# Kernel optimization log

Hardware: AMD Instinct MI355X
Metric: run time of the kernel (lower is better)

## Reference

```python
import jax, jax.numpy as jnp
import numpy as np

B_TREES, NARY, HS, NHEAD, NLVL = 16, 3, 512, 2, 6
EDIM = 352
LN_EPS = 1e-5

def _build_structure():
    # forest of B_TREES perfect ternary trees, depth NLVL; nodes numbered leaves-first, level-major
    off, o = {}, 0
    for l in range(NLVL - 1, -1, -1):
        off[l] = o
        o += B_TREES * 3 ** l
    node_ids = [off[l] + np.arange(B_TREES * 3 ** l) for l in range(NLVL)]
    child_idx = {}
    for l in range(NLVL - 1):
        m = 3 ** l
        t = np.repeat(np.arange(B_TREES), m)
        p = np.tile(np.arange(m), B_TREES)
        base = off[l + 1] + t * (3 ** (l + 1)) + 3 * p
        child_idx[l] = base[:, None] + np.arange(NARY)[None, :]
    return o, node_ids, child_idx

N_NODES, NODE_IDS, CHILD_IDX = _build_structure()

def _ln(x, w, b):
    mu = x.mean(-1, keepdims=True)
    var = x.var(-1, keepdims=True)
    return (x - mu) / jnp.sqrt(var + LN_EPS) * w + b

def _mha(x, wqkv, bqkv, wo, bo):
    # x: [S, B, H]; torch MHA with batch_first=False (seq dim 0, as in reduce_func)
    S, B, H = x.shape
    hd = H // NHEAD
    q, k, v = jnp.split(x @ wqkv.T + bqkv, 3, axis=-1)
    q = q.reshape(S, B, NHEAD, hd)
    k = k.reshape(S, B, NHEAD, hd)
    v = v.reshape(S, B, NHEAD, hd)
    scores = jnp.einsum('sbnd,tbnd->bnst', q, k) / jnp.sqrt(jnp.asarray(hd, x.dtype))
    attn = jax.nn.softmax(scores, axis=-1)
    o = jnp.einsum('bnst,tbnd->sbnd', attn, v).reshape(S, B, H)
    return o @ wo.T + bo

def _transformer(x, qkv_w, qkv_b, out_w, out_b, ln1_w, ln1_b, ff1_w, ff1_b, ff2_w, ff2_b, ln2_w, ln2_b):
    # 2 post-norm TransformerEncoderLayers, relu FF, dropout off (eval)
    for i in range(2):
        x = _ln(x + _mha(x, qkv_w[i], qkv_b[i], out_w[i], out_b[i]), ln1_w[i], ln1_b[i])
        ff = jax.nn.relu(x @ ff1_w[i].T + ff1_b[i]) @ ff2_w[i].T + ff2_b[i]
        x = _ln(x + ff, ln2_w[i], ln2_b[i])
    return x

def _forward(floats, ints):
    (user_emb, poi_emb, cat_emb, coo_emb, time_pos, W_iou, U_iou, b_iou,
     W_f, U_f, b_f, qkv_w, qkv_b, out_w, out_b, ln1_w, ln1_b, ff1_w, ff1_b,
     ff2_w, ff2_b, ln2_w, ln2_b, dec_poi_w, dec_poi_b, dec_cat_w, dec_cat_b,
     dec_coo_w, dec_coo_b) = floats
    user_ids, poi_ids, cat_ids, coo_ids, time_ids, mask = ints
    mi = mask.astype(jnp.int32)
    x = jnp.concatenate([user_emb[user_ids * mi], poi_emb[poi_ids * mi],
                         cat_emb[cat_ids * mi], coo_emb[coo_ids * mi]], axis=1)
    x = x + 0.5 * time_pos[time_ids * mi]
    x = x * mask.astype(x.dtype)[:, None]  # embed_dropout is identity in eval; per-node mask
    h = jnp.zeros((N_NODES, HS), x.dtype)
    c = jnp.zeros((N_NODES, HS), x.dtype)
    # leaves: reduce never fires -> iou stays at W_iou(x) (no b_iou), c = 0
    leaf = NODE_IDS[NLVL - 1]
    i0, o0, u0 = jnp.split(x[leaf] @ W_iou.T, 3, axis=1)
    c_leaf = jax.nn.sigmoid(i0) * jnp.tanh(u0)
    h = h.at[leaf].set(jax.nn.sigmoid(o0) * jnp.tanh(c_leaf))
    c = c.at[leaf].set(c_leaf)
    # topological propagation, bottom-up level frontiers
    for l in range(NLVL - 2, -1, -1):
        idx = NODE_IDS[l]
        ci = CHILD_IDX[l]
        m = idx.shape[0]
        h_ch = h[ci]  # mailbox gather [m, nary, HS]
        c_ch = c[ci]
        xl = x[idx]
        Wx = jnp.tile(xl @ W_f.T, (1, NARY))
        f = jax.nn.sigmoid(Wx + h_ch.reshape(m, NARY * HS) @ U_f.T + jnp.tile(b_f, (1, NARY)))
        h_att = _transformer(h_ch, qkv_w, qkv_b, out_w, out_b, ln1_w, ln1_b,
                             ff1_w, ff1_b, ff2_w, ff2_b, ln2_w, ln2_b)
        iou = xl @ W_iou.T + h_att.reshape(m, NARY * HS) @ U_iou.T + b_iou
        c_red = jnp.sum(f.reshape(m, NARY, HS) * c_ch, axis=1)
        i1, o1, u1 = jnp.split(iou, 3, axis=1)
        c_new = jax.nn.sigmoid(i1) * jnp.tanh(u1) + c_red
        h_new = jax.nn.sigmoid(o1) * jnp.tanh(c_new)
        h = h.at[idx].set(h_new)
        c = c.at[idx].set(c_new)
    # model_dropout identity in eval
    y_poi = h @ dec_poi_w.T + dec_poi_b
    y_cat = h @ dec_cat_w.T + dec_cat_b
    y_coo = h @ dec_coo_w.T + dec_coo_b
    return y_poi, y_cat, y_coo

def setup_inputs():
    key = jax.random.key(0)
    ks = iter(jax.random.split(key, 64))
    def rn(shape, s=0.05):
        return jax.random.normal(next(ks), shape, dtype=jnp.float32) * s
    def ri(shape, hi):
        return jax.random.randint(next(ks), shape, 0, hi, dtype=jnp.int32)
    N = N_NODES
    return dict(
        user_ids=ri([N], 3000), poi_ids=ri([N], 5000), cat_ids=ri([N], 300),
        coo_ids=ri([N], 1024), time_ids=ri([N], 96), mask=ri([N], 2),
        user_emb=rn([3000, 128], 0.02), poi_emb=rn([5000, 128], 0.02),
        cat_emb=rn([300, 32], 0.02), coo_emb=rn([1024, 64], 0.02),
        time_pos=rn([96, EDIM], 0.02),
        W_iou=rn([3 * HS, EDIM]), U_iou=rn([3 * HS, NARY * HS]), b_iou=jnp.zeros((1, 3 * HS)),
        W_f=rn([HS, EDIM]), U_f=rn([NARY * HS, NARY * HS]), b_f=jnp.zeros((1, HS)),
        qkv_w=rn([2, 3 * HS, HS]), qkv_b=jnp.zeros((2, 3 * HS)),
        out_w=rn([2, HS, HS]), out_b=jnp.zeros((2, HS)),
        ln1_w=jnp.ones((2, HS)), ln1_b=jnp.zeros((2, HS)),
        ff1_w=rn([2, HS, HS]), ff1_b=jnp.zeros((2, HS)),
        ff2_w=rn([2, HS, HS]), ff2_b=jnp.zeros((2, HS)),
        ln2_w=jnp.ones((2, HS)), ln2_b=jnp.zeros((2, HS)),
        dec_poi_w=rn([5000, HS]), dec_poi_b=jnp.zeros((5000,)),
        dec_cat_w=rn([300, HS]), dec_cat_b=jnp.zeros((300,)),
        dec_coo_w=rn([1024, HS]), dec_coo_b=jnp.zeros((1024,)),
    )

def reference(user_ids, poi_ids, cat_ids, coo_ids, time_ids, mask,
              user_emb, poi_emb, cat_emb, coo_emb, time_pos,
              W_iou, U_iou, b_iou, W_f, U_f, b_f,
              qkv_w, qkv_b, out_w, out_b, ln1_w, ln1_b, ff1_w, ff1_b,
              ff2_w, ff2_b, ln2_w, ln2_b,
              dec_poi_w, dec_poi_b, dec_cat_w, dec_cat_b, dec_coo_w, dec_coo_b):
    floats = (user_emb, poi_emb, cat_emb, coo_emb, time_pos, W_iou, U_iou, b_iou,
              W_f, U_f, b_f, qkv_w, qkv_b, out_w, out_b, ln1_w, ln1_b, ff1_w, ff1_b,
              ff2_w, ff2_b, ln2_w, ln2_b, dec_poi_w, dec_poi_b, dec_cat_w, dec_cat_b,
              dec_coo_w, dec_coo_b)
    ints = (user_ids, poi_ids, cat_ids, coo_ids, time_ids, mask)
    return _forward(floats, ints)
```

## Files before the change

kernel.cpp:

```cpp
#include <hip/hip_runtime.h>
#include <hip/hip_bf16.h>


namespace {

constexpr int NN = 5824;
constexpr int ED = 352;

typedef __bf16 bf16;
typedef short s16x8 __attribute__((ext_vector_type(8)));
typedef float f32x4 __attribute__((ext_vector_type(4)));

__device__ __forceinline__ float sigmoidf_(float x) { return 1.f / (1.f + expf(-x)); }

__device__ __forceinline__ void gload_lds16(const void* g, void* s) {
  __builtin_amdgcn_global_load_lds(
      (const __attribute__((address_space(1))) unsigned int*)g,
      (__attribute__((address_space(3))) unsigned int*)s, 16, 0, 0);
}

template <int MODE, bool DUAL, bool BPAIR, bool BF32, bool PIPE>
__global__ __launch_bounds__(256) void bgemm_k(
    const bf16* __restrict__ A, const bf16* __restrict__ Alo,
    const bf16* __restrict__ Bh_, const bf16* __restrict__ Bl_,
    const float* __restrict__ Bf0, const float* __restrict__ Bf1,
    const float* __restrict__ Bf2,
    void* __restrict__ Cp, bf16* __restrict__ Clo, const float* __restrict__ Cacc,
    const float* __restrict__ bias, const float* __restrict__ bias1,
    const float* __restrict__ bias2, bf16* __restrict__ VTout, int mpad,
    int M, int N, int K, int lda, int ldb, int ldc, float alpha,
    long long sA1, long long sA2, long long sB1, long long sB2,
    long long sC1, long long sC2, int nh) {
  const int bz = blockIdx.z;
  const int b1 = bz / nh, b2 = bz - b1 * nh;
  A += (long long)b1 * sA1 + (long long)b2 * sA2;
  if (DUAL) Alo += (long long)b1 * sA1 + (long long)b2 * sA2;
  if (!BF32) {
    Bh_ += (long long)b1 * sB1 + (long long)b2 * sB2;
    if (BPAIR) Bl_ += (long long)b1 * sB1 + (long long)b2 * sB2;
  }
  const long long coff = (long long)b1 * sC1 + (long long)b2 * sC2;
  const int bm = blockIdx.y * 128, bn = blockIdx.x * 128;

  constexpr int NSTG = PIPE ? 2 : 1;
  __shared__ bf16 As[NSTG][128 * 32];
  __shared__ bf16 Ls[DUAL ? NSTG : 1][DUAL ? 128 * 32 : 8];
  __shared__ bf16 Bh[NSTG][128 * 32];
  __shared__ bf16 Bl[BPAIR ? NSTG : 1][BPAIR ? 128 * 32 : 8];
  const int tid = threadIdx.x;
  const int l = tid & 63;
  const int wr = ((tid >> 7) & 1) * 64;
  const int wc = ((tid >> 6) & 1) * 64;
  f32x4 acc[4][4];
#pragma unroll
  for (int i = 0; i < 4; ++i)
#pragma unroll
    for (int j = 0; j < 4; ++j) acc[i][j] = (f32x4){0.f, 0.f, 0.f, 0.f};

  auto STAGE = [&](int st, int k0) {
#pragma unroll
    for (int r = 0; r < 2; ++r) {
      int idx = r * 256 + tid;
      int row = idx >> 2, cs = idx & 3;
      int cg = cs ^ (row & 3);
      int ra = bm + row; if (ra > M - 1) ra = M - 1;
      int rb = bn + row; if (rb > N - 1) rb = N - 1;
      gload_lds16(A + (long long)ra * lda + k0 + cg * 8, &As[st][idx * 8]);
      if (DUAL) gload_lds16(Alo + (long long)ra * lda + k0 + cg * 8, &Ls[st][idx * 8]);
      if (BF32) {
        const float* src;
        if (rb < 5000)      src = Bf0 + (long long)rb * ldb + k0 + cg * 8;
        else if (rb < 5300) src = Bf1 + (long long)(rb - 5000) * ldb + k0 + cg * 8;
        else                src = Bf2 + (long long)(rb - 5300) * ldb + k0 + cg * 8;
        float4 x = *reinterpret_cast<const float4*>(src);
        float4 y = *reinterpret_cast<const float4*>(src + 4);
        float w[8] = {x.x, x.y, x.z, x.w, y.x, y.y, y.z, y.w};
        bf16 hb_[8], lb_[8];
#pragma unroll
        for (int q = 0; q < 8; ++q) {
          bf16 hq = (bf16)w[q];
          hb_[q] = hq;
          lb_[q] = (bf16)(w[q] - (float)hq);
        }
        *reinterpret_cast<s16x8*>(&Bh[st][idx * 8]) = *reinterpret_cast<s16x8*>(hb_);
        if (BPAIR)
          *reinterpret_cast<s16x8*>(&Bl[st][idx * 8]) = *reinterpret_cast<s16x8*>(lb_);
      } else {
        gload_lds16(Bh_ + (long long)rb * ldb + k0 + cg * 8, &Bh[st][idx * 8]);
        if (BPAIR) gload_lds16(Bl_ + (long long)rb * ldb + k0 + cg * 8, &Bl[st][idx * 8]);
      }
    }
  };

  auto COMPUTE = [&](int st) {
    s16x8 af[4], al[4], bh4[4], bl4[4];
#pragma unroll
    for (int mi = 0; mi < 4; ++mi) {
      int row = wr + mi * 16 + (l & 15);
      int ch = ((l >> 4) ^ row) & 3;
      af[mi] = *reinterpret_cast<const s16x8*>(&As[st][row * 32 + ch * 8]);
      if (DUAL) al[mi] = *reinterpret_cast<const s16x8*>(&Ls[st][row * 32 + ch * 8]);
    }
#pragma unroll
    for (int ni = 0; ni < 4; ++ni) {
      int row = wc + ni * 16 + (l & 15);
      int ch = ((l >> 4) ^ row) & 3;
      bh4[ni] = *reinterpret_cast<const s16x8*>(&Bh[st][row * 32 + ch * 8]);
      if (BPAIR) bl4[ni] = *reinterpret_cast<const s16x8*>(&Bl[st][row * 32 + ch * 8]);
    }
#pragma unroll
    for (int mi = 0; mi < 4; ++mi)
#pragma unroll
      for (int ni = 0; ni < 4; ++ni) {
        acc[mi][ni] =
            __builtin_amdgcn_mfma_f32_16x16x32_bf16(af[mi], bh4[ni], acc[mi][ni], 0, 0, 0);
        if (BPAIR)
          acc[mi][ni] =
              __builtin_amdgcn_mfma_f32_16x16x32_bf16(af[mi], bl4[ni], acc[mi][ni], 0, 0, 0);
        if (DUAL)
          acc[mi][ni] =
              __builtin_amdgcn_mfma_f32_16x16x32_bf16(al[mi], bh4[ni], acc[mi][ni], 0, 0, 0);
      }
  };

  if (!PIPE) {
    for (int k0 = 0; k0 < K; k0 += 32) {
      STAGE(0, k0);
      __syncthreads();
      COMPUTE(0);
      __syncthreads();
    }
  } else {
    STAGE(0, 0);
    asm volatile("s_waitcnt vmcnt(0)" ::: "memory");
    __builtin_amdgcn_s_barrier();
    int cur = 0;
    for (int k0 = 0; k0 < K; k0 += 32) {
      if (k0 + 32 < K) STAGE(cur ^ 1, k0 + 32);
      COMPUTE(cur);
      asm volatile("s_waitcnt vmcnt(0)" ::: "memory");
      __builtin_amdgcn_sched_barrier(0);
      __builtin_amdgcn_s_barrier();
      cur ^= 1;
    }
  }

  const int lc = l & 15, lr4 = (l >> 4) * 4;
#pragma unroll
  for (int mi = 0; mi < 4; ++mi) {
#pragma unroll
    for (int j = 0; j < 4; ++j) {
      int r = bm + wr + mi * 16 + lr4 + j;
      if (MODE != 7 && r >= M) continue;
#pragma unroll
      for (int ni = 0; ni < 4; ++ni) {
        int c = bn + wc + ni * 16 + lc;
        if (c >= N) continue;
        float v = alpha * acc[mi][ni][j];
        if (MODE == 6) {
          v += (c < 5000) ? bias[c] : (c < 5300) ? bias1[c - 5000] : bias2[c - 5300];
        } else if (bias) {
          v += bias[c];
        }
        long long idx = coff + (long long)r * ldc + c;
        if (MODE == 7) {
          if (c >= 1024 && r < 3 * mpad) {
            bf16 pv = (r < M) ? (bf16)v : (bf16)0.f;
            int r3 = r % 3, s = r / 3;
            int hh = (c - 1024) >> 8, n = (c - 1024) & 255;
            VTout[(long long)((r3 * 2 + hh) * 256 + n) * mpad + s] = pv;
          }
          if (r < M) ((bf16*)Cp)[idx] = (bf16)v;
        } else if (MODE == 5) {
          ((float*)Cp)[idx] = v + Cacc[idx];
        } else if (MODE == 0) {
          ((float*)Cp)[idx] = v;
        } else if (MODE == 3) {
          ((bf16*)Cp)[idx] = (bf16)v;
        } else if (MODE == 4) {
          v = fmaxf(v, 0.f);
          bf16 hv = (bf16)v;
          ((bf16*)Cp)[idx] = hv;
          Clo[idx] = (bf16)(v - (float)hv);
        } else {
          float* o0 = (float*)Cp;
          if (c < 5000)      o0[(long long)r * 5000 + c] = v;
          else if (c < 5300) o0[29120000LL + (long long)r * 300 + (c - 5000)] = v;
          else               o0[30867200LL + (long long)r * 1024 + (c - 5300)] = v;
        }
      }
    }
  }
}

static void bgemm(hipStream_t st, int mode, bool dual, bool bpair,
                  const bf16* A, const bf16* Alo, const bf16* Bh, const bf16* Bl,
                  void* Cp, bf16* Clo, const float* Cacc,
                  const float* bias, const float* bias1, const float* bias2,
                  bf16* VTout, int mpad,
                  int M, int N, int K, int lda, int ldb, int ldc, float alpha,
                  int batches = 1, long long sA1 = 0, long long sA2 = 0,
                  long long sB1 = 0, long long sB2 = 0, long long sC1 = 0,
                  long long sC2 = 0, int nh = 1,
                  const float* Bf0 = nullptr, const float* Bf1 = nullptr,
                  const float* Bf2 = nullptr, bool bf32 = false) {
  dim3 g((N + 127) / 128, (M + 127) / 128, batches), b(256);
  long long nblocks = (long long)g.x * g.y * g.z;
  const bool pipe = (!bf32) && (mode != 6) && nblocks <= 1024;
#define BGL(MD_, DU_, BP_, BFF_, PP_)                                                    \
  bgemm_k<MD_, DU_, BP_, BFF_, PP_><<<g, b, 0, st>>>(                                    \
      A, Alo, Bh, Bl, Bf0, Bf1, Bf2, Cp, Clo, Cacc, bias, bias1, bias2, VTout, mpad,     \
      M, N, K, lda, ldb, ldc, alpha, sA1, sA2, sB1, sB2, sC1, sC2, nh)
#define BGL2(MD_, DU_, BP_)                                                              \
  do { if (pipe) BGL(MD_, DU_, BP_, false, true); else BGL(MD_, DU_, BP_, false, false); \
  } while (0)
  if (mode == 0 && !dual && bpair)        BGL2(0, false, true);
  else if (mode == 0 && dual && bpair)    BGL2(0, true, true);
  else if (mode == 0 && !dual && !bpair)  BGL2(0, false, false);
  else if (mode == 3)                     BGL2(3, false, false);
  else if (mode == 4)                     BGL2(4, true, true);
  else if (mode == 5)                     BGL2(5, true, true);
  else if (mode == 6 && !bf32)            BGL(6, false, false, false, false);
  else if (mode == 6 && bf32)             BGL(6, false, false, true, false);
  else                                    BGL2(7, true, true);
#undef BGL2
#undef BGL
}

struct SegArgs {
  const float* src[8];
  bf16* hi[8];
  bf16* lo[8];
  int start[9];
};
__global__ __launch_bounds__(256) void split_k(SegArgs a, int total8) {
  for (int i = blockIdx.x * 256 + threadIdx.x; i < total8; i += gridDim.x * 256) {
    int s = 0;
    while (i >= a.start[s + 1]) ++s;
    long long off = (long long)(i - a.start[s]) * 8;
    const float4* p = reinterpret_cast<const float4*>(a.src[s] + off);
    float4 x = p[0], y = p[1];
    float w[8] = {x.x, x.y, x.z, x.w, y.x, y.y, y.z, y.w};
    bf16 hb[8], lb[8];
#pragma unroll
    for (int q = 0; q < 8; ++q) {
      bf16 hq = (bf16)w[q];
      hb[q] = hq;
      lb[q] = (bf16)(w[q] - (float)hq);
    }
    *reinterpret_cast<s16x8*>(a.hi[s] + off) = *reinterpret_cast<s16x8*>(hb);
    if (a.lo[s]) *reinterpret_cast<s16x8*>(a.lo[s] + off) = *reinterpret_cast<s16x8*>(lb);
  }
}

__global__ __launch_bounds__(256) void embed_k(
    const int* __restrict__ uid, const int* __restrict__ pid, const int* __restrict__ cid,
    const int* __restrict__ gid, const int* __restrict__ tmid, const int* __restrict__ mask,
    const float* __restrict__ ue, const float* __restrict__ pe, const float* __restrict__ ce,
    const float* __restrict__ ge, const float* __restrict__ tp, bf16* __restrict__ xb) {
  int e = blockIdx.x * 256 + threadIdx.x;
  if (e >= NN * ED) return;
  int n = e / ED, j = e - n * ED;
  int mi = mask[n];
  float fm = (float)mi;
  float v;
  if (j < 128)      v = ue[(long long)(uid[n] * mi) * 128 + j];
  else if (j < 256) v = pe[(long long)(pid[n] * mi) * 128 + (j - 128)];
  else if (j < 288) v = ce[(long long)(cid[n] * mi) * 32 + (j - 256)];
  else              v = ge[(long long)(gid[n] * mi) * 64 + (j - 288)];
  v += 0.5f * tp[(long long)(tmid[n] * mi) * ED + j];
  xb[e] = (bf16)(v * fm);
}

__global__ __launch_bounds__(256) void fcred_k(
    const float* __restrict__ wxa, const float* __restrict__ ufh,
    const float* __restrict__ bf_, const float* __restrict__ c, float* __restrict__ cred,
    int m, int cbase, int tl, int woff) {
  int e = blockIdx.x * 256 + threadIdx.x;
  if (e >= m * 512) return;
  int r = e >> 9, d = e & 511;
  float w = wxa[(long long)(woff + r) * 512 + d] + bf_[d];
  int t = r / tl, p = r - t * tl;
  long long cb = (long long)(cbase + t * 3 * tl + 3 * p) * 512 + d;
  long long ub = (long long)r * 1536;
  float acc = 0.f;
#pragma unroll
  for (int k = 0; k < 3; ++k) {
    float f = sigmoidf_(w + ufh[ub + k * 512 + d]);
    acc += f * c[cb + (long long)k * 512];
  }
  cred[e] = acc;
}

__global__ __launch_bounds__(256) void combine_k(
    const float* __restrict__ iou, const float* __restrict__ cred, float* __restrict__ c,
    bf16* __restrict__ hhi, bf16* __restrict__ hlo, int off, int m, int tl3, int tlp,
    bf16* __restrict__ nxthi, bf16* __restrict__ nxtlo) {
  int e = blockIdx.x * 256 + threadIdx.x;
  if (e >= m * 512) return;
  int r = e >> 9, d = e & 511;
  long long b = (long long)r * 1536;
  float iv = iou[b + d], ov = iou[b + 512 + d], uv = iou[b + 1024 + d];
  float cr = cred ? cred[e] : 0.f;
  float cn = sigmoidf_(iv) * tanhf(uv) + cr;
  float hn = sigmoidf_(ov) * tanhf(cn);
  long long o = (long long)(off + r) * 512 + d;
  c[o] = cn;
  bf16 hv = (bf16)hn;
  bf16 lo = (bf16)(hn - (float)hv);
  hhi[o] = hv;
  hlo[o] = lo;
  if (nxthi) {
    int t = r / tl3, q = r - t * tl3;
    int qp = q / 3, slot = q - 3 * qp;
    long long dst = (long long)(t * tlp + qp) * 1536 + slot * 512 + d;
    nxthi[dst] = hv;
    nxtlo[dst] = lo;
  }
}

__global__ __launch_bounds__(256) void ln_k(
    const bf16* __restrict__ ahi, const bf16* __restrict__ alo, const float* __restrict__ b,
    const float* __restrict__ w, const float* __restrict__ bias,
    bf16* __restrict__ ohi, bf16* __restrict__ olo) {
  int r = blockIdx.x, t = threadIdx.x;
  long long base = (long long)r * 512;
  float v0 = (float)ahi[base + t] + (float)alo[base + t] + b[base + t];
  float v1 = (float)ahi[base + 256 + t] + (float)alo[base + 256 + t] + b[base + 256 + t];
  __shared__ float s1[256], s2[256];
  s1[t] = v0 + v1;
  s2[t] = v0 * v0 + v1 * v1;
  __syncthreads();
  for (int s = 128; s > 0; s >>= 1) {
    if (t < s) { s1[t] += s1[t + s]; s2[t] += s2[t + s]; }
    __syncthreads();
  }
  float mu = s1[0] * (1.f / 512.f);
  float var = s2[0] * (1.f / 512.f) - mu * mu;
  float rs = rsqrtf(var + 1e-5f);
  float o0 = (v0 - mu) * rs * w[t] + bias[t];
  float o1 = (v1 - mu) * rs * w[256 + t] + bias[256 + t];
  bf16 h0 = (bf16)o0, h1 = (bf16)o1;
  ohi[base + t] = h0;       olo[base + t] = (bf16)(o0 - (float)h0);
  ohi[base + 256 + t] = h1; olo[base + 256 + t] = (bf16)(o1 - (float)h1);
}

__global__ __launch_bounds__(256) void softmax_pb_k(float* __restrict__ sc, int m, int mpad) {
  long long r = blockIdx.x;
  float* row = sc + r * (long long)m;
  bf16* prow = (bf16*)sc + r * (long long)(2 * m);
  int t = threadIdx.x;
  __shared__ float sh[256];
  float mx = -3.4e38f;
  for (int j = t; j < m; j += 256) mx = fmaxf(mx, row[j]);
  sh[t] = mx;
  __syncthreads();
  for (int s = 128; s > 0; s >>= 1) {
    if (t < s) sh[t] = fmaxf(sh[t], sh[t + s]);
    __syncthreads();
  }
  mx = sh[0];
  __syncthreads();
  float ev[6];
  float sum = 0.f;
  int cnt = 0;
  for (int j = t; j < m; j += 256) {
    float e = expf(row[j] - mx);
    ev[cnt++] = e;
    sum += e;
  }
  sh[t] = sum;
  __syncthreads();
  for (int s = 128; s > 0; s >>= 1) {
    if (t < s) sh[t] += sh[t + s];
    __syncthreads();
  }
  float inv = 1.f / sh[0];
  cnt = 0;
  for (int j = t; j < m; j += 256) prow[j] = (bf16)(ev[cnt++] * inv);
  for (int j = m + t; j < mpad; j += 256) prow[j] = (bf16)0.f;
}

}

extern "C" void kernel_launch(void* const* d_in, const int* in_sizes, int n_in,
                              void* d_out, int out_size, void* d_ws, size_t ws_size,
                              hipStream_t stream) {
  const int* uid  = (const int*)d_in[0];
  const int* pid  = (const int*)d_in[1];
  const int* cid  = (const int*)d_in[2];
  const int* gid  = (const int*)d_in[3];
  const int* tmid = (const int*)d_in[4];
  const int* mask = (const int*)d_in[5];
  const float* ue = (const float*)d_in[6];
  const float* pe = (const float*)d_in[7];
  const float* ce = (const float*)d_in[8];
  const float* ge = (const float*)d_in[9];
  const float* tp = (const float*)d_in[10];
  const float* b_iou = (const float*)d_in[13];
  const float* b_f = (const float*)d_in[16];
  const float* qkv_b = (const float*)d_in[18];
  const float* out_b = (const float*)d_in[20];
  const float* ln1_w = (const float*)d_in[21];
  const float* ln1_b = (const float*)d_in[22];
  const float* ff1_b = (const float*)d_in[24];
  const float* ff2_b = (const float*)d_in[26];
  const float* ln2_w = (const float*)d_in[27];
  const float* ln2_b = (const float*)d_in[28];
  const float* dpw = (const float*)d_in[29];
  const float* dpb = (const float*)d_in[30];
  const float* dcw = (const float*)d_in[31];
  const float* dcb = (const float*)d_in[32];
  const float* dgw = (const float*)d_in[33];
  const float* dgb = (const float*)d_in[34];

  float* ws = (float*)d_ws;
  bf16* Hhi = (bf16*)ws;
  bf16* Hlo = Hhi + 2981888LL;
  float* Cc = ws + 2981888LL;
  bf16* DhiW = (bf16*)(ws + 5963776LL);
  const bool wsfit = ws_size >= 30330880ULL;

  float* ob = (float*)d_out;
  float* IOUa = ob;
  float* WXa  = ob + 8945664LL;
  float* CRED = ob + 9936896LL;
  bf16* RAhi  = (bf16*)(ob + 10600448LL);
  bf16* RAlo  = RAhi + 1990656LL;
  bf16* RBhi  = (bf16*)(ob + 12591104LL);
  bf16* RBlo  = RBhi + 1990656LL;
  bf16* UP    = (bf16*)(ob + 14581760LL);
  bf16* TE    = (bf16*)(ob + 19300352LL);
  float* TB   = ob + 22446080LL;

  bf16* Uihi = UP;
  bf16* Uilo = UP + 2359296LL;
  bf16* Ufhi = UP + 4718592LL;
  bf16* Uflo = UP + 7077888LL;
  bf16* qkvhi = TE;
  bf16* qkvlo = TE + 1572864LL;
  bf16* outhi = TE + 3145728LL;
  bf16* outlo = TE + 3670016LL;
  bf16* ff1hi = TE + 4194304LL;
  bf16* ff1lo = TE + 4718592LL;
  bf16* ff2hi = TE + 5242880LL;
  bf16* ff2lo = TE + 5767168LL;

  float* SC   = TB;
  float* PQ   = TB + 10077696LL;
  bf16* VT    = (bf16*)(TB + 13063680LL);
  bf16* Xb    = (bf16*)TB;
  bf16* WP    = (bf16*)(TB + 1025024LL);
  bf16* Wihi  = WP;
  bf16* Wilo  = WP + 540672LL;
  bf16* Wfhi  = WP + 1081344LL;
  bf16* Wflo  = WP + 1261568LL;

  float* UFH  = PQ;
  bf16* QKVb  = (bf16*)PQ;
  bf16* ATTOb = (bf16*)PQ;
  float* XB   = TB;
  bf16* XChi  = (bf16*)(TB + 1990656LL);
  bf16* XClo  = (bf16*)(TB + 2985984LL);

  {
    SegArgs a{};
    const int n8[8] = {294912, 294912, 196608, 65536, 65536, 65536, 67584, 22528};
    a.src[0] = (const float*)d_in[12]; a.hi[0] = Uihi;  a.lo[0] = Uilo;
    a.src[1] = (const float*)d_in[15]; a.hi[1] = Ufhi;  a.lo[1] = Uflo;
    a.src[2] = (const float*)d_in[17]; a.hi[2] = qkvhi; a.lo[2] = qkvlo;
    a.src[3] = (const float*)d_in[19]; a.hi[3] = outhi; a.lo[3] = outlo;
    a.src[4] = (const float*)d_in[23]; a.hi[4] = ff1hi; a.lo[4] = ff1lo;
    a.src[5] = (const float*)d_in[25]; a.hi[5] = ff2hi; a.lo[5] = ff2lo;
    a.src[6] = (const float*)d_in[11]; a.hi[6] = Wihi;  a.lo[6] = Wilo;
    a.src[7] = (const float*)d_in[14]; a.hi[7] = Wfhi;  a.lo[7] = Wflo;
    a.start[0] = 0;
    for (int i = 0; i < 8; ++i) a.start[i + 1] = a.start[i] + n8[i];
    int total8 = a.start[8];
    int blocks = (total8 + 255) / 256; if (blocks > 4096) blocks = 4096;
    split_k<<<blocks, 256, 0, stream>>>(a, total8);
    if (wsfit) {
      SegArgs d{};
      const int dn8[3] = {320000, 19200, 65536};
      d.src[0] = dpw; d.hi[0] = DhiW;             d.lo[0] = nullptr;
      d.src[1] = dcw; d.hi[1] = DhiW + 2560000LL; d.lo[1] = nullptr;
      d.src[2] = dgw; d.hi[2] = DhiW + 2713600LL; d.lo[2] = nullptr;
      d.start[0] = 0;
      for (int i = 0; i < 3; ++i) d.start[i + 1] = d.start[i] + dn8[i];
      for (int i = 3; i < 8; ++i) d.start[i + 1] = d.start[3];
      int dt8 = d.start[3];
      int db = (dt8 + 255) / 256; if (db > 4096) db = 4096;
      split_k<<<db, 256, 0, stream>>>(d, dt8);
    }
  }

  embed_k<<<(NN * ED + 255) / 256, 256, 0, stream>>>(uid, pid, cid, gid, tmid, mask,
                                                     ue, pe, ce, ge, tp, Xb);

  bgemm(stream, 0, false, true, Xb, nullptr, Wihi, Wilo, IOUa, nullptr, nullptr,
        nullptr, nullptr, nullptr, nullptr, 0, NN, 1536, 352, 352, 352, 1536, 1.f);
  bgemm(stream, 0, false, true, Xb + 3888LL * ED, nullptr, Wfhi, Wflo, WXa, nullptr,
        nullptr, nullptr, nullptr, nullptr, nullptr, 0, 1936, 512, 352, 352, 352, 512, 1.f);

  combine_k<<<(3888 * 512 + 255) / 256, 256, 0, stream>>>(
      IOUa, nullptr, Cc, Hhi, Hlo, 0, 3888, 243, 81, RAhi, RAlo);

  static const int OFFL[6] = {5808, 5760, 5616, 5184, 3888, 0};
  int tl = 81;
  for (int l = 4; l >= 0; --l, tl /= 3) {
    int m = 16 * tl;
    int off = OFFL[l];
    int cbase = OFFL[l + 1];
    int T = 3 * m;
    int mpad = (m + 31) & ~31;

    bgemm(stream, 0, true, true, RAhi, RAlo, Ufhi, Uflo, UFH, nullptr, nullptr,
          nullptr, nullptr, nullptr, nullptr, 0, m, 1536, 1536, 1536, 1536, 1536, 1.f);
    fcred_k<<<(m * 512 + 255) / 256, 256, 0, stream>>>(WXa, UFH, b_f, Cc, CRED,
                                                       m, cbase, tl, off - 3888);

    bf16 *curhi = RAhi, *curlo = RAlo, *nxthi = RBhi, *nxtlo = RBlo;
    for (int i = 0; i < 2; ++i) {
      bgemm(stream, 7, true, true, curhi, curlo, qkvhi + (long long)i * 786432,
            qkvlo + (long long)i * 786432, QKVb, nullptr, nullptr,
            qkv_b + i * 1536, nullptr, nullptr, VT, mpad,
            T, 1536, 512, 512, 512, 1536, 1.f);
      bgemm(stream, 0, false, false, QKVb, nullptr, QKVb + 512, nullptr, SC, nullptr,
            nullptr, nullptr, nullptr, nullptr, nullptr, 0,
            m, m, 256, 4608, 4608, m, 0.0625f,
            6, 1536, 256, 1536, 256, 2LL * m * m, (long long)m * m, 2);
      softmax_pb_k<<<6 * m, 256, 0, stream>>>(SC, m, mpad);
      bgemm(stream, 3, false, false, (bf16*)SC, nullptr, VT, nullptr, ATTOb, nullptr,
            nullptr, nullptr, nullptr, nullptr, nullptr, 0,
            m, 256, mpad, 2 * m, mpad, 1536, 1.f,
            6, 4LL * m * m, 2LL * m * m, 2LL * 256 * mpad, 256LL * mpad, 512, 256, 2);
      bgemm(stream, 0, false, true, ATTOb, nullptr, outhi + (long long)i * 262144,
            outlo + (long long)i * 262144, XB, nullptr, nullptr,
            out_b + i * 512, nullptr, nullptr, nullptr, 0,
            T, 512, 512, 512, 512, 512, 1.f);
      ln_k<<<T, 256, 0, stream>>>(curhi, curlo, XB, ln1_w + i * 512, ln1_b + i * 512,
                                  nxthi, nxtlo);
      bgemm(stream, 4, true, true, nxthi, nxtlo, ff1hi + (long long)i * 262144,
            ff1lo + (long long)i * 262144, XChi, XClo, nullptr,
            ff1_b + i * 512, nullptr, nullptr, nullptr, 0,
            T, 512, 512, 512, 512, 512, 1.f);
      bgemm(stream, 0, true, true, XChi, XClo, ff2hi + (long long)i * 262144,
            ff2lo + (long long)i * 262144, XB, nullptr, nullptr,
            ff2_b + i * 512, nullptr, nullptr, nullptr, 0,
            T, 512, 512, 512, 512, 512, 1.f);
      ln_k<<<T, 256, 0, stream>>>(nxthi, nxtlo, XB, ln2_w + i * 512, ln2_b + i * 512,
                                  curhi, curlo);
    }

    bgemm(stream, 5, true, true, curhi, curlo, Uihi, Uilo,
          IOUa + (long long)off * 1536, nullptr, IOUa + (long long)off * 1536,
          b_iou, nullptr, nullptr, nullptr, 0, m, 1536, 1536, 1536, 1536, 1536, 1.f);
    combine_k<<<(m * 512 + 255) / 256, 256, 0, stream>>>(
        IOUa + (long long)off * 1536, CRED, Cc, Hhi, Hlo, off, m, tl, tl / 3,
        l > 0 ? RAhi : nullptr, l > 0 ? RAlo : nullptr);
  }

  if (wsfit) {
    bgemm(stream, 6, false, false, Hhi, nullptr, DhiW, nullptr, ob, nullptr, nullptr,
          dpb, dcb, dgb, nullptr, 0, NN, 6324, 512, 512, 512, 0, 1.f);
  } else {
    bgemm(stream, 6, false, false, Hhi, nullptr, nullptr, nullptr, ob, nullptr, nullptr,
          dpb, dcb, dgb, nullptr, 0, NN, 6324, 512, 512, 512, 0, 1.f,
          1, 0, 0, 0, 0, 0, 0, 1, dpw, dcw, dgw, true);
  }
}
```

Baseline: 2.562 ms.

## Fuse attention score GEMM, softmax and PV GEMM into flash-attention kernel

Replaces the three-step attention (score GEMM into an fp32 buffer, row softmax writing bf16 probabilities, then a PV GEMM) with one online-softmax kernel. Each block holds a 128-query tile and streams 128-key tiles through LDS with MFMA, keeping running max and sum. This avoids writing and rereading the m×m score matrix for the large tree levels and removes two launches. In exchange the QK^T product is recomputed for each of the two V-column halves, and the buffers are moved to new workspace offsets.

```diff
diff --git a/kernel.cpp b/kernel.cpp
--- a/kernel.cpp
+++ b/kernel.cpp
@@ -175,8 +175,6 @@
           ((float*)Cp)[idx] = v + Cacc[idx];
         } else if (MODE == 0) {
           ((float*)Cp)[idx] = v;
-        } else if (MODE == 3) {
-          ((bf16*)Cp)[idx] = (bf16)v;
         } else if (MODE == 4) {
           v = fmaxf(v, 0.f);
           bf16 hv = (bf16)v;
@@ -216,8 +214,6 @@
   } while (0)
   if (mode == 0 && !dual && bpair)        BGL2(0, false, true);
   else if (mode == 0 && dual && bpair)    BGL2(0, true, true);
-  else if (mode == 0 && !dual && !bpair)  BGL2(0, false, false);
-  else if (mode == 3)                     BGL2(3, false, false);
   else if (mode == 4)                     BGL2(4, true, true);
   else if (mode == 5)                     BGL2(5, true, true);
   else if (mode == 6 && !bf32)            BGL(6, false, false, false, false);
@@ -225,6 +221,177 @@
   else                                    BGL2(7, true, true);
 #undef BGL2
 #undef BGL
+}
+
+__global__ __launch_bounds__(256) void fattn_k(
+    const bf16* __restrict__ qkv, const bf16* __restrict__ vt,
+    bf16* __restrict__ out, int m, int mpad) {
+  const int q0 = blockIdx.x * 128;
+  const int zz = blockIdx.y;
+  const int z = zz >> 1, half = zz & 1;
+  const int b = z >> 1, h = z & 1;
+  const bf16* Q = qkv + (long long)b * 1536 + h * 256;
+  const bf16* Kp = Q + 512;
+  const bf16* Vh = vt + ((long long)z * 256 + half * 128) * mpad;
+
+  __shared__ bf16 SAB[256 * 32];
+  __shared__ bf16 Pl[128 * 136];
+  __shared__ float rred[2][128];
+  __shared__ float mrow[128], lrow[128], newm[128], rs[128];
+
+  const int tid = threadIdx.x;
+  const int l = tid & 63;
+  const int wr = ((tid >> 7) & 1) * 64;
+  const int wc = ((tid >> 6) & 1) * 64;
+  const int wcH = wc >> 6;
+
+  f32x4 acc_o[4][4];
+#pragma unroll
+  for (int i = 0; i < 4; ++i)
+#pragma unroll
+    for (int j = 0; j < 4; ++j) acc_o[i][j] = (f32x4){0.f, 0.f, 0.f, 0.f};
+  if (tid < 128) { mrow[tid] = -3.4e38f; lrow[tid] = 0.f; }
+  __syncthreads();
+
+  const int ntiles = (m + 127) / 128;
+  for (int t = 0; t < ntiles; ++t) {
+    const int kv0 = t * 128;
+    f32x4 acc_s[4][4];
+#pragma unroll
+    for (int i = 0; i < 4; ++i)
+#pragma unroll
+      for (int j = 0; j < 4; ++j) acc_s[i][j] = (f32x4){0.f, 0.f, 0.f, 0.f};
+    for (int k0 = 0; k0 < 256; k0 += 32) {
+#pragma unroll
+      for (int r = 0; r < 2; ++r) {
+        int idx = r * 256 + tid;
+        int row = idx >> 2, cs = idx & 3;
+        int cg = cs ^ (row & 3);
+        int qr = q0 + row; if (qr > m - 1) qr = m - 1;
+        int kr = kv0 + row; if (kr > m - 1) kr = m - 1;
+        gload_lds16(Q + (long long)qr * 4608 + k0 + cg * 8, &SAB[idx * 8]);
+        gload_lds16(Kp + (long long)kr * 4608 + k0 + cg * 8, &SAB[4096 + idx * 8]);
+      }
+      __syncthreads();
+      s16x8 af[4], bh4[4];
+#pragma unroll
+      for (int mi = 0; mi < 4; ++mi) {
+        int row = wr + mi * 16 + (l & 15);
+        int ch = ((l >> 4) ^ row) & 3;
+        af[mi] = *reinterpret_cast<const s16x8*>(&SAB[row * 32 + ch * 8]);
+      }
+#pragma unroll
+      for (int ni = 0; ni < 4; ++ni) {
+        int row = wc + ni * 16 + (l & 15);
+        int ch = ((l >> 4) ^ row) & 3;
+        bh4[ni] = *reinterpret_cast<const s16x8*>(&SAB[4096 + row * 32 + ch * 8]);
+      }
+#pragma unroll
+      for (int mi = 0; mi < 4; ++mi)
+#pragma unroll
+        for (int ni = 0; ni < 4; ++ni)
+          acc_s[mi][ni] =
+              __builtin_amdgcn_mfma_f32_16x16x32_bf16(af[mi], bh4[ni], acc_s[mi][ni], 0, 0, 0);
+      __syncthreads();
+    }
+#pragma unroll
+    for (int mi = 0; mi < 4; ++mi)
+#pragma unroll
+      for (int jj = 0; jj < 4; ++jj) {
+        float v = -3.4e38f;
+#pragma unroll
+        for (int ni = 0; ni < 4; ++ni) v = fmaxf(v, acc_s[mi][ni][jj]);
+        v *= 0.0625f;
+        v = fmaxf(v, __shfl_xor(v, 1));
+        v = fmaxf(v, __shfl_xor(v, 2));
+        v = fmaxf(v, __shfl_xor(v, 4));
+        v = fmaxf(v, __shfl_xor(v, 8));
+        if ((l & 15) == 0) rred[wcH][wr + mi * 16 + (l >> 4) * 4 + jj] = v;
+      }
+    __syncthreads();
+    if (tid < 128) {
+      float tm = fmaxf(rred[0][tid], rred[1][tid]);
+      float mo = mrow[tid];
+      float mn = fmaxf(mo, tm);
+      newm[tid] = mn;
+      float r = expf(mo - mn);
+      rs[tid] = r;
+      mrow[tid] = mn;
+      lrow[tid] *= r;
+    }
+    __syncthreads();
+#pragma unroll
+    for (int mi = 0; mi < 4; ++mi)
+#pragma unroll
+      for (int jj = 0; jj < 4; ++jj) {
+        int row = wr + mi * 16 + (l >> 4) * 4 + jj;
+        float mn = newm[row];
+        float r = rs[row];
+        float s = 0.f;
+#pragma unroll
+        for (int ni = 0; ni < 4; ++ni) {
+          int col = wc + ni * 16 + (l & 15);
+          float p = (kv0 + col < m) ? expf(acc_s[mi][ni][jj] * 0.0625f - mn) : 0.f;
+          Pl[row * 136 + col] = (bf16)p;
+          s += p;
+          acc_o[mi][ni][jj] *= r;
+        }
+        s += __shfl_xor(s, 1);
+        s += __shfl_xor(s, 2);
+        s += __shfl_xor(s, 4);
+        s += __shfl_xor(s, 8);
+        if ((l & 15) == 0) rred[wcH][row] = s;
+      }
+    __syncthreads();
+    if (tid < 128) lrow[tid] += rred[0][tid] + rred[1][tid];
+    int klim = m - kv0; if (klim > 128) klim = 128;
+    for (int k0 = 0; k0 < klim; k0 += 32) {
+#pragma unroll
+      for (int r = 0; r < 2; ++r) {
+        int idx = r * 256 + tid;
+        int row = idx >> 2, cs = idx & 3;
+        int cg = cs ^ (row & 3);
+        int col = kv0 + k0 + cg * 8;
+        if (col > mpad - 8) col = mpad - 8;
+        gload_lds16(Vh + (long long)row * mpad + col, &SAB[idx * 8]);
+      }
+      __syncthreads();
+      s16x8 pf[4], vf[4];
+#pragma unroll
+      for (int mi = 0; mi < 4; ++mi) {
+        int pr = wr + mi * 16 + (l & 15);
+        pf[mi] = *reinterpret_cast<const s16x8*>(&Pl[pr * 136 + k0 + (l >> 4) * 8]);
+      }
+#pragma unroll
+      for (int ni = 0; ni < 4; ++ni) {
+        int vr = wc + ni * 16 + (l & 15);
+        int ch = ((l >> 4) ^ vr) & 3;
+        vf[ni] = *reinterpret_cast<const s16x8*>(&SAB[vr * 32 + ch * 8]);
+      }
+#pragma unroll
+      for (int mi = 0; mi < 4; ++mi)
+#pragma unroll
+        for (int ni = 0; ni < 4; ++ni)
+          acc_o[mi][ni] =
+              __builtin_amdgcn_mfma_f32_16x16x32_bf16(pf[mi], vf[ni], acc_o[mi][ni], 0, 0, 0);
+      __syncthreads();
+    }
+  }
+  __syncthreads();
+#pragma unroll
+  for (int mi = 0; mi < 4; ++mi)
+#pragma unroll
+    for (int jj = 0; jj < 4; ++jj) {
+      int row = wr + mi * 16 + (l >> 4) * 4 + jj;
+      int gr = q0 + row;
+      if (gr >= m) continue;
+      float linv = 1.f / lrow[row];
+#pragma unroll
+      for (int ni = 0; ni < 4; ++ni) {
+        int n = half * 128 + wc + ni * 16 + (l & 15);
+        out[(long long)gr * 1536 + b * 512 + h * 256 + n] = (bf16)(acc_o[mi][ni][jj] * linv);
+      }
+    }
 }
 
 struct SegArgs {
@@ -343,42 +510,6 @@
   bf16 h0 = (bf16)o0, h1 = (bf16)o1;
   ohi[base + t] = h0;       olo[base + t] = (bf16)(o0 - (float)h0);
   ohi[base + 256 + t] = h1; olo[base + 256 + t] = (bf16)(o1 - (float)h1);
-}
-
-__global__ __launch_bounds__(256) void softmax_pb_k(float* __restrict__ sc, int m, int mpad) {
-  long long r = blockIdx.x;
-  float* row = sc + r * (long long)m;
-  bf16* prow = (bf16*)sc + r * (long long)(2 * m);
-  int t = threadIdx.x;
-  __shared__ float sh[256];
-  float mx = -3.4e38f;
-  for (int j = t; j < m; j += 256) mx = fmaxf(mx, row[j]);
-  sh[t] = mx;
-  __syncthreads();
-  for (int s = 128; s > 0; s >>= 1) {
-    if (t < s) sh[t] = fmaxf(sh[t], sh[t + s]);
-    __syncthreads();
-  }
-  mx = sh[0];
-  __syncthreads();
-  float ev[6];
-  float sum = 0.f;
-  int cnt = 0;
-  for (int j = t; j < m; j += 256) {
-    float e = expf(row[j] - mx);
-    ev[cnt++] = e;
-    sum += e;
-  }
-  sh[t] = sum;
-  __syncthreads();
-  for (int s = 128; s > 0; s >>= 1) {
-    if (t < s) sh[t] += sh[t + s];
-    __syncthreads();
-  }
-  float inv = 1.f / sh[0];
-  cnt = 0;
-  for (int j = t; j < m; j += 256) prow[j] = (bf16)(ev[cnt++] * inv);
-  for (int j = m + t; j < mpad; j += 256) prow[j] = (bf16)0.f;
 }
 
 }
@@ -446,7 +577,10 @@
   bf16* ff2hi = TE + 5242880LL;
   bf16* ff2lo = TE + 5767168LL;
 
-  float* SC   = TB;
+  bf16* ATTOb = (bf16*)TB;
+  float* XB   = TB + 995328LL;
+  bf16* XChi  = (bf16*)(TB + 1990656LL);
+  bf16* XClo  = (bf16*)(TB + 2985984LL);
   float* PQ   = TB + 10077696LL;
   bf16* VT    = (bf16*)(TB + 13063680LL);
   bf16* Xb    = (bf16*)TB;
@@ -458,10 +592,6 @@
 
   float* UFH  = PQ;
   bf16* QKVb  = (bf16*)PQ;
-  bf16* ATTOb = (bf16*)PQ;
-  float* XB   = TB;
-  bf16* XChi  = (bf16*)(TB + 1990656LL);
-  bf16* XClo  = (bf16*)(TB + 2985984LL);
 
   {
     SegArgs a{};
@@ -525,15 +655,10 @@
             qkvlo + (long long)i * 786432, QKVb, nullptr, nullptr,
             qkv_b + i * 1536, nullptr, nullptr, VT, mpad,
             T, 1536, 512, 512, 512, 1536, 1.f);
-      bgemm(stream, 0, false, false, QKVb, nullptr, QKVb + 512, nullptr, SC, nullptr,
-            nullptr, nullptr, nullptr, nullptr, nullptr, 0,
-            m, m, 256, 4608, 4608, m, 0.0625f,
-            6, 1536, 256, 1536, 256, 2LL * m * m, (long long)m * m, 2);
-      softmax_pb_k<<<6 * m, 256, 0, stream>>>(SC, m, mpad);
-      bgemm(stream, 3, false, false, (bf16*)SC, nullptr, VT, nullptr, ATTOb, nullptr,
-            nullptr, nullptr, nullptr, nullptr, nullptr, 0,
-            m, 256, mpad, 2 * m, mpad, 1536, 1.f,
-            6, 4LL * m * m, 2LL * m * m, 2LL * 256 * mpad, 256LL * mpad, 512, 256, 2);
+      {
+        int ntiles = (m + 127) / 128;
+        fattn_k<<<dim3(ntiles, 12), 256, 0, stream>>>(QKVb, VT, ATTOb, m, mpad);
+      }
       bgemm(stream, 0, false, true, ATTOb, nullptr, outhi + (long long)i * 262144,
             outlo + (long long)i * 262144, XB, nullptr, nullptr,
             out_b + i * 512, nullptr, nullptr, nullptr, 0,
```

Measured after the change: 2.798 ms. 9.2% more time.
